# Kernel tuning notes

Hardware: AMD Instinct MI355X
Metric: run time of the kernel (lower is better)

Reference implementation:

```python
import jax, jax.numpy as jnp
import numpy as np

N = 100000
E = 3200000
B = 128
IN_C, HID, OUT_C = 128, 64, 1


def setup_inputs() -> dict:
    key = jax.random.key(0)
    ks = jax.random.split(key, 12)
    x = jax.random.normal(ks[0], (N, IN_C), dtype=jnp.float32)
    edge_index = jax.random.randint(ks[1], (2, E), 0, N, dtype=jnp.int64)
    batch = jnp.sort(jax.random.randint(ks[2], (N,), 0, B, dtype=jnp.int64))
    def glorot(k, fi, fo):
        lim = np.sqrt(6.0 / (fi + fo))
        return jax.random.uniform(k, (fi, fo), jnp.float32, -lim, lim)
    return {
        "x": x,
        "edge_index": edge_index,
        "batch": batch,
        "W0": glorot(ks[3], IN_C, HID), "b0": jnp.zeros((HID,), jnp.float32),
        "W1": glorot(ks[4], HID, HID), "b1": jnp.zeros((HID,), jnp.float32),
        "W2": glorot(ks[5], HID, HID), "b2": jnp.zeros((HID,), jnp.float32),
        "Wm1": glorot(ks[6], HID, HID // 2), "bm1": jnp.zeros((HID // 2,), jnp.float32),
        "Wm2": glorot(ks[7], HID // 2, OUT_C), "bm2": jnp.zeros((OUT_C,), jnp.float32),
    }


def reference(x, edge_index, batch, W0, b0, W1, b1, W2, b2, Wm1, bm1, Wm2, bm2):
    # PyG GCNConv: add self-loops, symmetric deg^-1/2 normalization,
    # linear transform, scatter-add at target, then bias.
    loops = jnp.arange(N, dtype=edge_index.dtype)
    src = jnp.concatenate([edge_index[0], loops])  # (E+N,)
    dst = jnp.concatenate([edge_index[1], loops])
    deg = jax.ops.segment_sum(jnp.ones_like(dst, dtype=x.dtype), dst, num_segments=N)
    dis = jnp.where(deg > 0, jax.lax.rsqrt(deg), 0.0)  # deg^-1/2
    norm = (dis[src] * dis[dst])[:, None]  # (E+N, 1)

    def gcn(h, W, b):
        h = h @ W                                        # (N, HID)
        msg = h[src] * norm                              # gather + scale
        agg = jax.ops.segment_sum(msg, dst, num_segments=N)
        return agg + b

    h = jax.nn.relu(gcn(x, W0, b0))
    h = jax.nn.relu(gcn(h, W1, b1))   # dropout is identity in eval mode
    h = jax.nn.relu(gcn(h, W2, b2))

    # global_mean_pool over `batch` segment ids
    sums = jax.ops.segment_sum(h, batch, num_segments=B)          # (B, HID)
    cnts = jax.ops.segment_sum(jnp.ones((N,), h.dtype), batch, num_segments=B)
    pooled = sums / jnp.maximum(cnts, 1.0)[:, None]

    z = jax.nn.relu(pooled @ Wm1 + bm1)
    return z @ Wm2 + bm2  # (B, OUT_C)
```

## Files before the change

### kernel.cpp

```cpp
#include <hip/hip_runtime.h>
#include <hip/hip_fp16.h>

#define NN 100000
#define EE 3200000
#define BB 128
#define MM (EE + NN)
#define NBK 391
#define CHUNK 8192
#define NCH ((MM + CHUNK - 1) / CHUNK)


__global__ void k_init(int* __restrict__ bstart, int* __restrict__ bend,
                       int* __restrict__ gcnt) {
  int i = blockIdx.x * 256 + threadIdx.x;
  if (i < BB) { bstart[i] = 0; bend[i] = 0; }
  if (i < NBK) gcnt[i] = 0;
}

__global__ __launch_bounds__(256) void k_hist(const int* __restrict__ ei, int* __restrict__ gcnt) {
  __shared__ int lh[NBK];
  int t = threadIdx.x;
  for (int b = t; b < NBK; b += 256) lh[b] = 0;
  __syncthreads();
  int base = blockIdx.x * CHUNK;
  for (int i = t; i < CHUNK; i += 256) {
    int e = base + i; if (e >= MM) break;
    int d = (e < EE) ? ei[EE + e] : (e - EE);
    atomicAdd(&lh[d >> 8], 1);
  }
  __syncthreads();
  for (int b = t; b < NBK; b += 256) { int c = lh[b]; if (c) atomicAdd(&gcnt[b], c); }
}

__global__ void k_bscan(const int* __restrict__ gcnt, int* __restrict__ curB,
                        int* __restrict__ bktoff, int* __restrict__ rs) {
  __shared__ int sc[512];
  int t = threadIdx.x;
  int v = (t < NBK) ? gcnt[t] : 0;
  sc[t] = v; __syncthreads();
  for (int off = 1; off < 512; off <<= 1) {
    int u = (t >= off) ? sc[t - off] : 0;
    __syncthreads();
    sc[t] += u;
    __syncthreads();
  }
  int ex = sc[t] - v;
  if (t < NBK) curB[t] = ex;
  if (t <= NBK) bktoff[t] = ex;
  if (t == 0) rs[NN] = MM;
}

__global__ __launch_bounds__(256) void k_scatter(const int* __restrict__ ei,
                                                 int* __restrict__ curB, int2* __restrict__ bkt) {
  __shared__ int lh[NBK];
  __shared__ int lbase[NBK];
  int t = threadIdx.x;
  for (int b = t; b < NBK; b += 256) lh[b] = 0;
  __syncthreads();
  int base = blockIdx.x * CHUNK;
  for (int i = t; i < CHUNK; i += 256) {
    int e = base + i; if (e >= MM) break;
    int d = (e < EE) ? ei[EE + e] : (e - EE);
    atomicAdd(&lh[d >> 8], 1);
  }
  __syncthreads();
  for (int b = t; b < NBK; b += 256) {
    int c = lh[b];
    lbase[b] = c ? atomicAdd(&curB[b], c) : 0;
    lh[b] = 0;
  }
  __syncthreads();
  for (int i = t; i < CHUNK; i += 256) {
    int e = base + i; if (e >= MM) break;
    int s, d;
    if (e < EE) { s = ei[e]; d = ei[EE + e]; } else { s = e - EE; d = s; }
    int b = d >> 8;
    int r = atomicAdd(&lh[b], 1);
    bkt[lbase[b] + r] = make_int2(s, d);
  }
}

__global__ __launch_bounds__(256) void k_bucket(const int2* __restrict__ bkt,
                                                const int* __restrict__ bktoff,
                                                float* __restrict__ dis, int* __restrict__ rs,
                                                int* __restrict__ srcs) {
  int b = blockIdx.x, t = threadIdx.x;
  int start = bktoff[b], end = bktoff[b + 1];
  int nbase = b << 8;
  __shared__ int cnt[256];
  __shared__ int scn[256];
  __shared__ int curs[256];
  cnt[t] = 0;
  __syncthreads();
  for (int i = start + t; i < end; i += 256)
    atomicAdd(&cnt[bkt[i].y - nbase], 1);
  __syncthreads();
  int v = cnt[t];
  scn[t] = v; __syncthreads();
  for (int off = 1; off < 256; off <<= 1) {
    int u = (t >= off) ? scn[t - off] : 0;
    __syncthreads();
    scn[t] += u;
    __syncthreads();
  }
  int excl = scn[t] - v;
  int node = nbase + t;
  if (node < NN) {
    rs[node] = start + excl;
    dis[node] = rsqrtf((float)v);
  }
  curs[t] = start + excl;
  __syncthreads();
  for (int i = start + t; i < end; i += 256) {
    int2 e = bkt[i];
    int pos = atomicAdd(&curs[e.y - nbase], 1);
    srcs[pos] = e.x;
  }
}

__global__ void k_bounds(const int* __restrict__ batch, int* __restrict__ bstart,
                         int* __restrict__ bend) {
  int i = blockIdx.x * 256 + threadIdx.x;
  if (i >= NN) return;
  int b = batch[i];
  if (i == 0 || batch[i - 1] != b) bstart[b] = i;
  if (i == NN - 1 || batch[i + 1] != b) bend[b] = i + 1;
}


template <int CIN>
__global__ __launch_bounds__(256) void k_matmul_scale(
    const float* __restrict__ in, const float* __restrict__ W,
    const float* __restrict__ dis, ushort* __restrict__ out) {
  __shared__ float Wl[CIN * 64];
  __shared__ float xr[64 * 68];
  int t = threadIdx.x;
  for (int i = t * 4; i < CIN * 64; i += 1024)
    *(float4*)&Wl[i] = *(const float4*)&W[i];

  int base = blockIdx.x * 64;
  int rows = NN - base; if (rows > 64) rows = 64;

  int cg = t & 15, rg = t >> 4;
  int c0 = cg * 4;
  float acc[4][4] = {};

  for (int kh = 0; kh < CIN; kh += 64) {
    for (int i = t * 4; i < rows * 64; i += 1024) {
      int r = i >> 6, c = i & 63;
      *(float4*)&xr[r * 68 + c] = *(const float4*)&in[(base + r) * CIN + kh + c];
    }
    __syncthreads();
#pragma unroll
    for (int kl = 0; kl < 64; kl += 4) {
      float4 xv[4], wv[4];
#pragma unroll
      for (int j = 0; j < 4; j++) xv[j] = *(float4*)&xr[(rg * 4 + j) * 68 + kl];
#pragma unroll
      for (int kk = 0; kk < 4; kk++) wv[kk] = *(float4*)&Wl[(kh + kl + kk) * 64 + c0];
#pragma unroll
      for (int kk = 0; kk < 4; kk++) {
#pragma unroll
        for (int j = 0; j < 4; j++) {
          float xs = (&xv[j].x)[kk];
          acc[j][0] += xs * wv[kk].x;
          acc[j][1] += xs * wv[kk].y;
          acc[j][2] += xs * wv[kk].z;
          acc[j][3] += xs * wv[kk].w;
        }
      }
    }
    __syncthreads();
  }

#pragma unroll
  for (int j = 0; j < 4; j++) {
    int r = base + rg * 4 + j;
    if (r < NN) {
      float dv = dis[r];
      ushort4 o;
      o.x = __half_as_ushort(__float2half_rn(acc[j][0] * dv));
      o.y = __half_as_ushort(__float2half_rn(acc[j][1] * dv));
      o.z = __half_as_ushort(__float2half_rn(acc[j][2] * dv));
      o.w = __half_as_ushort(__float2half_rn(acc[j][3] * dv));
      *(ushort4*)&out[r * 64 + c0] = o;
    }
  }
}


__global__ __launch_bounds__(256) void k_agg(
    const ushort* __restrict__ tp, const int* __restrict__ row_start,
    const int* __restrict__ srcs, const float* __restrict__ dis,
    const float* __restrict__ bias, float* __restrict__ out) {
  int wid = (blockIdx.x * 256 + threadIdx.x) >> 6;
  int lane = threadIdx.x & 63;
  if (wid >= NN) return;
  int s = row_start[wid], e = row_start[wid + 1];
  float a0 = 0.f, a1 = 0.f, a2 = 0.f, a3 = 0.f;
  float a4 = 0.f, a5 = 0.f, a6 = 0.f, a7 = 0.f;
  int p = s;
  for (; p + 8 <= e; p += 8) {
    int i0 = srcs[p],     i1 = srcs[p + 1], i2 = srcs[p + 2], i3 = srcs[p + 3];
    int i4 = srcs[p + 4], i5 = srcs[p + 5], i6 = srcs[p + 6], i7 = srcs[p + 7];
    a0 += __half2float(__ushort_as_half(tp[i0 * 64 + lane]));
    a1 += __half2float(__ushort_as_half(tp[i1 * 64 + lane]));
    a2 += __half2float(__ushort_as_half(tp[i2 * 64 + lane]));
    a3 += __half2float(__ushort_as_half(tp[i3 * 64 + lane]));
    a4 += __half2float(__ushort_as_half(tp[i4 * 64 + lane]));
    a5 += __half2float(__ushort_as_half(tp[i5 * 64 + lane]));
    a6 += __half2float(__ushort_as_half(tp[i6 * 64 + lane]));
    a7 += __half2float(__ushort_as_half(tp[i7 * 64 + lane]));
  }
  for (; p < e; ++p) a0 += __half2float(__ushort_as_half(tp[srcs[p] * 64 + lane]));
  float acc = ((a0 + a1) + (a2 + a3)) + ((a4 + a5) + (a6 + a7));
  float r = acc * dis[wid] + bias[lane];
  out[wid * 64 + lane] = fmaxf(r, 0.f);
}


__global__ __launch_bounds__(256) void k_pool_mlp(
    const float* __restrict__ h, const int* __restrict__ bstart, const int* __restrict__ bend,
    const float* __restrict__ Wm1, const float* __restrict__ bm1,
    const float* __restrict__ Wm2, const float* __restrict__ bm2,
    float* __restrict__ out) {
  int b = blockIdx.x;
  int t = threadIdx.x;
  int lane = t & 63, w = t >> 6;
  int s = bstart[b], e = bend[b];
  float acc = 0.f;
  for (int i = s + w; i < e; i += 4) acc += h[i * 64 + lane];
  __shared__ float sums[4][64];
  __shared__ float pooled[64];
  sums[w][lane] = acc;
  __syncthreads();
  if (t < 64) {
    float tot = sums[0][t] + sums[1][t] + sums[2][t] + sums[3][t];
    int cnt = e - s;
    pooled[t] = tot / fmaxf((float)cnt, 1.0f);
  }
  __syncthreads();
  if (t < 32) {
    float z = bm1[t];
#pragma unroll
    for (int c = 0; c < 64; c++) z += pooled[c] * Wm1[c * 32 + t];
    z = fmaxf(z, 0.f) * Wm2[t];
#pragma unroll
    for (int off = 16; off > 0; off >>= 1) z += __shfl_down(z, off, 32);
    if (t == 0) out[b] = z + bm2[0];
  }
}


extern "C" void kernel_launch(void* const* d_in, const int* in_sizes, int n_in,
                              void* d_out, int out_size, void* d_ws, size_t ws_size,
                              hipStream_t stream) {
  const float* x   = (const float*)d_in[0];
  const int*   ei  = (const int*)d_in[1];
  const int*   bat = (const int*)d_in[2];
  const float* W0  = (const float*)d_in[3];
  const float* b0  = (const float*)d_in[4];
  const float* W1  = (const float*)d_in[5];
  const float* b1  = (const float*)d_in[6];
  const float* W2  = (const float*)d_in[7];
  const float* b2  = (const float*)d_in[8];
  const float* Wm1 = (const float*)d_in[9];
  const float* bm1 = (const float*)d_in[10];
  const float* Wm2 = (const float*)d_in[11];
  const float* bm2 = (const float*)d_in[12];
  float* out = (float*)d_out;

  char* ws = (char*)d_ws;
  size_t off = 0;
  auto alloc = [&](size_t bytes) -> void* {
    void* p = ws + off; off += (bytes + 255) & ~(size_t)255; return p;
  };
  float*  dis    = (float*) alloc((size_t)NN * 4);
  int*    rs     = (int*)   alloc((size_t)(NN + 1) * 4);
  int*    srcs   = (int*)   alloc((size_t)MM * 4);
  void*   regA   = alloc((size_t)MM * 8);
  ushort* tp     = (ushort*)alloc((size_t)NN * 64 * 2);
  int*    bst    = (int*)   alloc(BB * 4);
  int*    ben    = (int*)   alloc(BB * 4);
  int*    gcnt   = (int*)   alloc(NBK * 4);
  int*    curB   = (int*)   alloc(NBK * 4);
  int*    bktoff = (int*)   alloc((NBK + 1) * 4);

  int2*  bkt = (int2*)regA;
  float* h   = (float*)regA;

  k_init<<<2, 256, 0, stream>>>(bst, ben, gcnt);
  k_hist<<<NCH, 256, 0, stream>>>(ei, gcnt);
  k_bscan<<<1, 512, 0, stream>>>(gcnt, curB, bktoff, rs);
  k_scatter<<<NCH, 256, 0, stream>>>(ei, curB, bkt);
  k_bucket<<<NBK, 256, 0, stream>>>(bkt, bktoff, dis, rs, srcs);
  k_bounds<<<(NN + 255) / 256, 256, 0, stream>>>(bat, bst, ben);

  const int mmgrid = (NN + 63) / 64;

  k_matmul_scale<128><<<mmgrid, 256, 0, stream>>>(x, W0, dis, tp);
  k_agg<<<(NN + 3) / 4, 256, 0, stream>>>(tp, rs, srcs, dis, b0, h);

  k_matmul_scale<64><<<mmgrid, 256, 0, stream>>>(h, W1, dis, tp);
  k_agg<<<(NN + 3) / 4, 256, 0, stream>>>(tp, rs, srcs, dis, b1, h);

  k_matmul_scale<64><<<mmgrid, 256, 0, stream>>>(h, W2, dis, tp);
  k_agg<<<(NN + 3) / 4, 256, 0, stream>>>(tp, rs, srcs, dis, b2, h);

  k_pool_mlp<<<BB, 256, 0, stream>>>(h, bst, ben, Wm1, bm1, Wm2, bm2, out);
}
```

Measured before the change: 648.5 us.

## Pack bucket entries into one int and gather two edges per wave in aggregation

The bucket sort now stores each edge as a single 32-bit word, with the source shifted left by 8 and the low 8 bits of the destination, instead of an int2. This halves the intermediate bucket traffic. The aggregation kernel now splits each wave into two halves that each gather a different neighbor row with 4-byte loads, two fp16 channels per lane. Indices are broadcast by shuffle from a single coalesced load, and the two halves are combined with a cross-half shuffle at the end. Packing relies on source ids fitting in 24 bits, which holds for N=100000.

```diff
diff --git a/kernel.cpp b/kernel.cpp
--- a/kernel.cpp
+++ b/kernel.cpp
@@ -51,7 +51,7 @@
 }
 
 __global__ __launch_bounds__(256) void k_scatter(const int* __restrict__ ei,
-                                                 int* __restrict__ curB, int2* __restrict__ bkt) {
+                                                 int* __restrict__ curB, int* __restrict__ bkt) {
   __shared__ int lh[NBK];
   __shared__ int lbase[NBK];
   int t = threadIdx.x;
@@ -76,11 +76,11 @@
     if (e < EE) { s = ei[e]; d = ei[EE + e]; } else { s = e - EE; d = s; }
     int b = d >> 8;
     int r = atomicAdd(&lh[b], 1);
-    bkt[lbase[b] + r] = make_int2(s, d);
-  }
-}
-
-__global__ __launch_bounds__(256) void k_bucket(const int2* __restrict__ bkt,
+    bkt[lbase[b] + r] = (s << 8) | (d & 255);
+  }
+}
+
+__global__ __launch_bounds__(256) void k_bucket(const int* __restrict__ bkt,
                                                 const int* __restrict__ bktoff,
                                                 float* __restrict__ dis, int* __restrict__ rs,
                                                 int* __restrict__ srcs) {
@@ -93,7 +93,7 @@
   cnt[t] = 0;
   __syncthreads();
   for (int i = start + t; i < end; i += 256)
-    atomicAdd(&cnt[bkt[i].y - nbase], 1);
+    atomicAdd(&cnt[bkt[i] & 255], 1);
   __syncthreads();
   int v = cnt[t];
   scn[t] = v; __syncthreads();
@@ -112,9 +112,9 @@
   curs[t] = start + excl;
   __syncthreads();
   for (int i = start + t; i < end; i += 256) {
-    int2 e = bkt[i];
-    int pos = atomicAdd(&curs[e.y - nbase], 1);
-    srcs[pos] = e.x;
+    int e = bkt[i];
+    int pos = atomicAdd(&curs[e & 255], 1);
+    srcs[pos] = ((unsigned)e) >> 8;
   }
 }
 
@@ -197,25 +197,47 @@
   int lane = threadIdx.x & 63;
   if (wid >= NN) return;
   int s = row_start[wid], e = row_start[wid + 1];
-  float a0 = 0.f, a1 = 0.f, a2 = 0.f, a3 = 0.f;
-  float a4 = 0.f, a5 = 0.f, a6 = 0.f, a7 = 0.f;
+  int half = lane >> 5;
+  int cp = lane & 31;
+  float ax[8] = {}, ay[8] = {};
+
   int p = s;
-  for (; p + 8 <= e; p += 8) {
-    int i0 = srcs[p],     i1 = srcs[p + 1], i2 = srcs[p + 2], i3 = srcs[p + 3];
-    int i4 = srcs[p + 4], i5 = srcs[p + 5], i6 = srcs[p + 6], i7 = srcs[p + 7];
-    a0 += __half2float(__ushort_as_half(tp[i0 * 64 + lane]));
-    a1 += __half2float(__ushort_as_half(tp[i1 * 64 + lane]));
-    a2 += __half2float(__ushort_as_half(tp[i2 * 64 + lane]));
-    a3 += __half2float(__ushort_as_half(tp[i3 * 64 + lane]));
-    a4 += __half2float(__ushort_as_half(tp[i4 * 64 + lane]));
-    a5 += __half2float(__ushort_as_half(tp[i5 * 64 + lane]));
-    a6 += __half2float(__ushort_as_half(tp[i6 * 64 + lane]));
-    a7 += __half2float(__ushort_as_half(tp[i7 * 64 + lane]));
-  }
-  for (; p < e; ++p) a0 += __half2float(__ushort_as_half(tp[srcs[p] * 64 + lane]));
-  float acc = ((a0 + a1) + (a2 + a3)) + ((a4 + a5) + (a6 + a7));
-  float r = acc * dis[wid] + bias[lane];
-  out[wid * 64 + lane] = fmaxf(r, 0.f);
+  for (; p + 16 <= e; p += 16) {
+    int idx = srcs[p + (lane & 15)];
+#pragma unroll
+    for (int j = 0; j < 8; j++) {
+      int r = __shfl(idx, 2 * j + half, 16);
+      uint u = *(const uint*)(tp + (((size_t)r) << 6) + (cp << 1));
+      ax[j] += __half2float(__ushort_as_half((ushort)(u & 0xffff)));
+      ay[j] += __half2float(__ushort_as_half((ushort)(u >> 16)));
+    }
+  }
+  for (; p + 2 <= e; p += 2) {
+    int r = srcs[p + half];
+    uint u = *(const uint*)(tp + (((size_t)r) << 6) + (cp << 1));
+    ax[0] += __half2float(__ushort_as_half((ushort)(u & 0xffff)));
+    ay[0] += __half2float(__ushort_as_half((ushort)(u >> 16)));
+  }
+  if (p < e && half == 0) {
+    int r = srcs[p];
+    uint u = *(const uint*)(tp + (((size_t)r) << 6) + (cp << 1));
+    ax[0] += __half2float(__ushort_as_half((ushort)(u & 0xffff)));
+    ay[0] += __half2float(__ushort_as_half((ushort)(u >> 16)));
+  }
+
+  float sx = ((ax[0] + ax[1]) + (ax[2] + ax[3])) + ((ax[4] + ax[5]) + (ax[6] + ax[7]));
+  float sy = ((ay[0] + ay[1]) + (ay[2] + ay[3])) + ((ay[4] + ay[5]) + (ay[6] + ay[7]));
+  sx += __shfl_xor(sx, 32);
+  sy += __shfl_xor(sy, 32);
+
+  if (half == 0) {
+    float dv = dis[wid];
+    float2 bv = *(const float2*)&bias[cp * 2];
+    float2 o;
+    o.x = fmaxf(sx * dv + bv.x, 0.f);
+    o.y = fmaxf(sy * dv + bv.y, 0.f);
+    *(float2*)&out[wid * 64 + cp * 2] = o;
+  }
 }
 
 
@@ -286,7 +308,7 @@
   int*    curB   = (int*)   alloc(NBK * 4);
   int*    bktoff = (int*)   alloc((NBK + 1) * 4);
 
-  int2*  bkt = (int2*)regA;
+  int*   bkt = (int*)regA;
   float* h   = (float*)regA;
 
   k_init<<<2, 256, 0, stream>>>(bst, ben, gcnt);
```

Result: faster. 607.1 us (-6.4%).
